# Performance work log

Measured on AMD Instinct MI355X. Metric: run time of the kernel, lower is better.

The kernel has to match this reference:

```python
import jax, jax.numpy as jnp
import numpy as np

NUM_HEADS = 8
HEAD_DIM = 64
GROUPS = 32
EPS = 1e-5


def setup_inputs() -> dict:
    key = jax.random.key(0)
    ks = jax.random.split(key, 7)
    B, C, H, W = 8, 512, 32, 32
    x = jax.random.normal(ks[0], (B, C, H, W), dtype=jnp.float32)
    gn_w = jnp.ones((C,), dtype=jnp.float32)
    gn_b = jnp.zeros((C,), dtype=jnp.float32)
    # 1x1 convs stored as [out, in] matrices
    qkv_w = jax.random.normal(ks[1], (3 * C, C), dtype=jnp.float32) * (1.0 / np.sqrt(C))
    qkv_b = jnp.zeros((3 * C,), dtype=jnp.float32)
    proj_w = jax.random.normal(ks[2], (C, C), dtype=jnp.float32) * (1.0 / np.sqrt(C))
    proj_b = jnp.zeros((C,), dtype=jnp.float32)
    return {"x": x, "gn_w": gn_w, "gn_b": gn_b, "qkv_w": qkv_w,
            "qkv_b": qkv_b, "proj_w": proj_w, "proj_b": proj_b}


def _group_norm(x, w, b):
    B, C, H, W = x.shape
    xg = x.reshape(B, GROUPS, C // GROUPS, H, W)
    mu = xg.mean(axis=(2, 3, 4), keepdims=True)
    var = xg.var(axis=(2, 3, 4), keepdims=True)
    xn = ((xg - mu) * jax.lax.rsqrt(var + EPS)).reshape(B, C, H, W)
    return xn * w[None, :, None, None] + b[None, :, None, None]


def reference(x, gn_w, gn_b, qkv_w, qkv_b, proj_w, proj_b):
    B, C, H, W = x.shape
    N = H * W
    h = _group_norm(x, gn_w, gn_b)
    # 1x1 conv == per-pixel matmul: [B, 3C, N]
    hf = h.reshape(B, C, N)
    qkv = jnp.einsum('oc,bcn->bon', qkv_w, hf) + qkv_b[None, :, None]
    qkv = qkv.reshape(B, 3, NUM_HEADS, HEAD_DIM, N)
    q, k, v = qkv[:, 0], qkv[:, 1], qkv[:, 2]  # each [B, h, d, N]
    attn = jnp.einsum('bhdi,bhdj->bhij', q, k) * (HEAD_DIM ** -0.5)
    attn = jax.nn.softmax(attn, axis=-1)
    out = jnp.einsum('bhij,bhdj->bhdi', attn, v)  # [B, h, d, N]
    out = out.reshape(B, C, N)
    out = jnp.einsum('oc,bcn->bon', proj_w, out) + proj_b[None, :, None]
    return x + out.reshape(B, C, H, W)
```

## Files before the change

### kernel.cpp

```cpp
#include <hip/hip_runtime.h>
#include <hip/hip_bf16.h>

#define BF16 __hip_bfloat16

typedef __attribute__((ext_vector_type(8))) short bf16x8;
typedef __attribute__((ext_vector_type(4))) float f32x4;
typedef __attribute__((ext_vector_type(4))) unsigned short ushort4v;
typedef __attribute__((ext_vector_type(4))) float float4v;

__device__ __forceinline__ unsigned short f2bf(float f) {
  BF16 h = __float2bfloat16(f);
  union { BF16 h; unsigned short u; } cv;
  cv.h = h;
  return cv.u;
}

__global__ __launch_bounds__(256) void cast_w_kernel(const float* __restrict__ qw,
                                                     const float* __restrict__ pw,
                                                     BF16* __restrict__ wq,
                                                     BF16* __restrict__ wp) {
  int i = blockIdx.x * 256 + threadIdx.x;
  if (i < 1536 * 512) wq[i] = __float2bfloat16(qw[i]);
  if (i < 512 * 512)  wp[i] = __float2bfloat16(pw[i]);
}

__global__ __launch_bounds__(256) void gn_kernel(const float* __restrict__ x,
                                                 const float* __restrict__ gw,
                                                 const float* __restrict__ gb,
                                                 BF16* __restrict__ h_t) {
  const int blk = blockIdx.x;
  const int bb = blk >> 5, g = blk & 31;
  const float* xg = x + (size_t)(bb * 512 + g * 16) * 1024;

  float s = 0.f, ss = 0.f;
  const float4v* x4 = (const float4v*)xg;
  for (int i = threadIdx.x; i < 4096; i += 256) {
    float4v v = x4[i];
    s  += v[0] + v[1] + v[2] + v[3];
    ss += v[0] * v[0] + v[1] * v[1] + v[2] * v[2] + v[3] * v[3];
  }
  for (int off = 32; off > 0; off >>= 1) {
    s  += __shfl_down(s, off, 64);
    ss += __shfl_down(ss, off, 64);
  }
  __shared__ float sred[8];
  const int wv = threadIdx.x >> 6;
  if ((threadIdx.x & 63) == 0) { sred[wv] = s; sred[4 + wv] = ss; }
  __syncthreads();
  const float S  = sred[0] + sred[1] + sred[2] + sred[3];
  const float SS = sred[4] + sred[5] + sred[6] + sred[7];
  const float mean = S * (1.f / 16384.f);
  const float var  = SS * (1.f / 16384.f) - mean * mean;
  const float rstd = rsqrtf(var + 1e-5f);

  const int ci = threadIdx.x & 15, nb = threadIdx.x >> 4;
  const int c  = g * 16 + ci;
  const float aw = gw[c] * rstd;
  const float ab = gb[c] - mean * aw;
  const float* xrow = xg + (size_t)ci * 1024;
  BF16* hb = h_t + (size_t)bb * 1024 * 512 + c;
  #pragma unroll 4
  for (int i = 0; i < 64; ++i) {
    int n = nb + i * 16;
    hb[(size_t)n * 512] = __float2bfloat16(aw * xrow[n] + ab);
  }
}

#define GEMM_PROLOGUE()                                                        \
  const int tid = threadIdx.x, l = tid & 63, wv = tid >> 6;                    \
  const int wm = wv >> 1, wn = wv & 1;                                         \
  const int lc = l & 15, lh = l >> 4;                                          \
  __shared__ BF16 Al[128 * 64];                                                \
  __shared__ BF16 Bl[128 * 64];                                                \
  f32x4 acc[4][4] = {};                                                        \
  for (int kt = 0; kt < 8; ++kt) {                                             \
    const int k0 = kt * 64;                                                    \
    __syncthreads();                                                           \
    _Pragma("unroll")                                                          \
    for (int it = 0; it < 4; ++it) {                                           \
      int sidx = it * 256 + tid;                                               \
      int row = sidx >> 3, cG = sidx & 7, cS = cG ^ (row & 7);                 \
      *(bf16x8*)&Al[(row * 8 + cS) * 8] =                                      \
          *(const bf16x8*)&A[(size_t)row * 512 + k0 + cG * 8];                 \
      *(bf16x8*)&Bl[(row * 8 + cS) * 8] =                                      \
          *(const bf16x8*)&B[(size_t)row * 512 + k0 + cG * 8];                 \
    }                                                                          \
    __syncthreads();                                                           \
    _Pragma("unroll")                                                          \
    for (int ks = 0; ks < 2; ++ks) {                                           \
      bf16x8 af[4], bfr[4];                                                    \
      _Pragma("unroll")                                                        \
      for (int i = 0; i < 4; ++i) {                                            \
        int rA = wm * 64 + i * 16 + lc;                                        \
        int cA = (ks * 4 + lh) ^ (rA & 7);                                     \
        af[i] = *(const bf16x8*)&Al[(rA * 8 + cA) * 8];                        \
        int rB = wn * 64 + i * 16 + lc;                                        \
        int cB = (ks * 4 + lh) ^ (rB & 7);                                     \
        bfr[i] = *(const bf16x8*)&Bl[(rB * 8 + cB) * 8];                       \
      }                                                                        \
      _Pragma("unroll")                                                        \
      for (int i = 0; i < 4; ++i)                                              \
        _Pragma("unroll")                                                      \
        for (int j = 0; j < 4; ++j)                                            \
          acc[i][j] = __builtin_amdgcn_mfma_f32_16x16x32_bf16(af[i], bfr[j],   \
                                                              acc[i][j], 0, 0, 0); \
    }                                                                          \
  }

__global__ __launch_bounds__(256) void qkv_gemm_kernel(const BF16* __restrict__ Wq,
                                                       const BF16* __restrict__ Ht,
                                                       const float* __restrict__ bias,
                                                       BF16* __restrict__ q_t,
                                                       BF16* __restrict__ k_t,
                                                       BF16* __restrict__ v_nat) {
  const int nt = blockIdx.x, mt = blockIdx.y, b = blockIdx.z;
  const int m0 = mt * 128, n0 = nt * 128;
  const BF16* A = Wq + (size_t)m0 * 512;
  const BF16* B = Ht + (size_t)b * 1024 * 512 + (size_t)n0 * 512;
  GEMM_PROLOGUE()

  const int r0 = lh * 4;
  #pragma unroll
  for (int mi = 0; mi < 4; ++mi) {
    const int o = m0 + wm * 64 + mi * 16 + r0;
    #pragma unroll
    for (int ni = 0; ni < 4; ++ni) {
      const int pix = n0 + wn * 64 + ni * 16 + lc;
      f32x4 a = acc[mi][ni];
      if (mt < 8) {
        const float scale = (mt < 4) ? 0.125f : 1.0f;
        const int hh = (o >> 6) & 7;
        const int d = o & 63;
        BF16* dst = (mt < 4 ? q_t : k_t) +
                    ((size_t)(b * 8 + hh) * 1024 + pix) * 64 + d;
        ushort4v pk;
        #pragma unroll
        for (int r = 0; r < 4; ++r) pk[r] = f2bf((a[r] + bias[o + r]) * scale);
        *(ushort4v*)dst = pk;
      } else {
        #pragma unroll
        for (int r = 0; r < 4; ++r) {
          const int vr = o + r - 1024;
          v_nat[((size_t)(b * 512 + vr)) * 1024 + pix] =
              __float2bfloat16(a[r] + bias[o + r]);
        }
      }
    }
  }
}

__global__ __launch_bounds__(256) void proj_gemm_kernel(const BF16* __restrict__ Wp,
                                                        const BF16* __restrict__ At,
                                                        const float* __restrict__ bias,
                                                        const float* __restrict__ x,
                                                        float* __restrict__ out) {
  const int nt = blockIdx.x, mt = blockIdx.y, b = blockIdx.z;
  const int m0 = mt * 128, n0 = nt * 128;
  const BF16* A = Wp + (size_t)m0 * 512;
  const BF16* B = At + (size_t)b * 1024 * 512 + (size_t)n0 * 512;
  GEMM_PROLOGUE()

  const int r0 = lh * 4;
  #pragma unroll
  for (int mi = 0; mi < 4; ++mi) {
    #pragma unroll
    for (int ni = 0; ni < 4; ++ni) {
      const int n = n0 + wn * 64 + ni * 16 + lc;
      f32x4 a = acc[mi][ni];
      #pragma unroll
      for (int r = 0; r < 4; ++r) {
        const int c = m0 + wm * 64 + mi * 16 + r0 + r;
        const size_t idx = ((size_t)(b * 512 + c)) * 1024 + n;
        out[idx] = x[idx] + bias[c] + a[r];
      }
    }
  }
}

__global__ __launch_bounds__(256) void attn_kernel(const BF16* __restrict__ q_t,
                                                   const BF16* __restrict__ k_t,
                                                   const BF16* __restrict__ v_nat,
                                                   BF16* __restrict__ attout) {
  const int bh = blockIdx.y;
  const int b = bh >> 3, hh = bh & 7;
  const int i0 = blockIdx.x * 64;
  const int tid = threadIdx.x, l = tid & 63, wv = tid >> 6;
  const int lc = l & 15, lh = l >> 4;

  __shared__ __align__(16) BF16 Kl[64 * 64];
  __shared__ __align__(16) BF16 Vl[64 * 64];
  __shared__ __align__(16) BF16 Pl[4][16][72];

  bf16x8 aq0, aq1;
  {
    const BF16* qp = q_t + ((size_t)bh * 1024 + i0 + wv * 16 + lc) * 64;
    aq0 = *(const bf16x8*)&qp[lh * 8];
    aq1 = *(const bf16x8*)&qp[32 + lh * 8];
  }

  f32x4 O[4] = {};
  float mrow[4], lrow[4];
  #pragma unroll
  for (int r = 0; r < 4; ++r) { mrow[r] = -1e30f; lrow[r] = 0.f; }

  const BF16* kbase = k_t + (size_t)bh * 1024 * 64;
  const BF16* vbase = v_nat + (size_t)bh * 64 * 1024;

  for (int jt = 0; jt < 16; ++jt) {
    const int j0 = jt * 64;
    __syncthreads();
    #pragma unroll
    for (int it = 0; it < 2; ++it) {
      int sidx = it * 256 + tid;
      int row = sidx >> 3, cG = sidx & 7, cS = cG ^ (row & 7);
      *(bf16x8*)&Kl[(row * 8 + cS) * 8] =
          *(const bf16x8*)&kbase[((size_t)(j0 + row)) * 64 + cG * 8];
      *(bf16x8*)&Vl[(row * 8 + cS) * 8] =
          *(const bf16x8*)&vbase[(size_t)row * 1024 + j0 + cG * 8];
    }
    __syncthreads();

    f32x4 Sv[4];
    #pragma unroll
    for (int jf = 0; jf < 4; ++jf) {
      f32x4 sacc = {};
      const int jl = jf * 16 + lc;
      {
        int cS = lh ^ (jl & 7);
        bf16x8 bk = *(const bf16x8*)&Kl[(jl * 8 + cS) * 8];
        sacc = __builtin_amdgcn_mfma_f32_16x16x32_bf16(aq0, bk, sacc, 0, 0, 0);
        cS = (4 + lh) ^ (jl & 7);
        bk = *(const bf16x8*)&Kl[(jl * 8 + cS) * 8];
        sacc = __builtin_amdgcn_mfma_f32_16x16x32_bf16(aq1, bk, sacc, 0, 0, 0);
      }
      Sv[jf] = sacc;
    }

    float pr[4][4];
    #pragma unroll
    for (int r = 0; r < 4; ++r) {
      float tmax = fmaxf(fmaxf(Sv[0][r], Sv[1][r]), fmaxf(Sv[2][r], Sv[3][r]));
      tmax = fmaxf(tmax, __shfl_xor(tmax, 1, 64));
      tmax = fmaxf(tmax, __shfl_xor(tmax, 2, 64));
      tmax = fmaxf(tmax, __shfl_xor(tmax, 4, 64));
      tmax = fmaxf(tmax, __shfl_xor(tmax, 8, 64));
      const float mnew = fmaxf(mrow[r], tmax);
      const float sc = __expf(mrow[r] - mnew);
      mrow[r] = mnew;
      float rs = 0.f;
      #pragma unroll
      for (int jf = 0; jf < 4; ++jf) {
        float p = __expf(Sv[jf][r] - mnew);
        pr[jf][r] = p;
        rs += p;
      }
      rs += __shfl_xor(rs, 1, 64);
      rs += __shfl_xor(rs, 2, 64);
      rs += __shfl_xor(rs, 4, 64);
      rs += __shfl_xor(rs, 8, 64);
      lrow[r] = lrow[r] * sc + rs;
      #pragma unroll
      for (int nf = 0; nf < 4; ++nf) O[nf][r] *= sc;
    }

    #pragma unroll
    for (int jf = 0; jf < 4; ++jf)
      #pragma unroll
      for (int r = 0; r < 4; ++r)
        Pl[wv][4 * lh + r][jf * 16 + lc] = __float2bfloat16(pr[jf][r]);

    const bf16x8 ap0 = *(const bf16x8*)&Pl[wv][lc][lh * 8];
    const bf16x8 ap1 = *(const bf16x8*)&Pl[wv][lc][32 + lh * 8];
    #pragma unroll
    for (int nf = 0; nf < 4; ++nf) {
      const int dl = nf * 16 + lc;
      int cS = lh ^ (dl & 7);
      bf16x8 bv = *(const bf16x8*)&Vl[(dl * 8 + cS) * 8];
      O[nf] = __builtin_amdgcn_mfma_f32_16x16x32_bf16(ap0, bv, O[nf], 0, 0, 0);
      cS = (4 + lh) ^ (dl & 7);
      bv = *(const bf16x8*)&Vl[(dl * 8 + cS) * 8];
      O[nf] = __builtin_amdgcn_mfma_f32_16x16x32_bf16(ap1, bv, O[nf], 0, 0, 0);
    }
  }

  #pragma unroll
  for (int r = 0; r < 4; ++r) {
    const float inv = 1.0f / lrow[r];
    const int irow = i0 + wv * 16 + 4 * lh + r;
    BF16* dst = attout + ((size_t)b * 1024 + irow) * 512 + hh * 64;
    #pragma unroll
    for (int nf = 0; nf < 4; ++nf)
      dst[nf * 16 + lc] = __float2bfloat16(O[nf][r] * inv);
  }
}

extern "C" void kernel_launch(void* const* d_in, const int* in_sizes, int n_in,
                              void* d_out, int out_size, void* d_ws, size_t ws_size,
                              hipStream_t stream) {
  const float* x      = (const float*)d_in[0];
  const float* gn_w   = (const float*)d_in[1];
  const float* gn_b   = (const float*)d_in[2];
  const float* qkv_w  = (const float*)d_in[3];
  const float* qkv_b  = (const float*)d_in[4];
  const float* proj_w = (const float*)d_in[5];
  const float* proj_b = (const float*)d_in[6];
  float* out = (float*)d_out;

  char* ws = (char*)d_ws;
  BF16* wq    = (BF16*)(ws);
  BF16* wp    = (BF16*)(ws + 1572864);
  BF16* h_t   = (BF16*)(ws + 2097152);
  BF16* q_t   = (BF16*)(ws + 10485760);
  BF16* k_t   = (BF16*)(ws + 18874368);
  BF16* v_nat = (BF16*)(ws + 27262976);
  BF16* attout = h_t;

  cast_w_kernel<<<3072, 256, 0, stream>>>(qkv_w, proj_w, wq, wp);
  gn_kernel<<<256, 256, 0, stream>>>(x, gn_w, gn_b, h_t);
  qkv_gemm_kernel<<<dim3(8, 12, 8), 256, 0, stream>>>(wq, h_t, qkv_b, q_t, k_t, v_nat);
  attn_kernel<<<dim3(16, 64), 256, 0, stream>>>(q_t, k_t, v_nat, attout);
  proj_gemm_kernel<<<dim3(8, 4, 8), 256, 0, stream>>>(wp, attout, proj_b, x, out);
}
```

Measured before the change: 194.0 us.

## Double-buffer attention K/V via direct global-to-LDS loads and transpose MFMA operands

GEMM and attention tile loads now use global_load_lds to write straight into LDS with the XOR swizzle applied on the global address side, skipping the register round-trip. The attention kernel double-buffers K/V so the next tile is fetched while the current one is computed. It also swaps MFMA operand order so each lane owns a whole query row: softmax needs fewer cross-lane shuffles and P and the output are written as packed 4-element stores. Risks are the ordering of the async LDS loads relative to the single barrier per iteration, and raising MFMA priority with s_setprio.

```diff
diff --git a/kernel.cpp b/kernel.cpp
--- a/kernel.cpp
+++ b/kernel.cpp
@@ -13,6 +13,12 @@
   union { BF16 h; unsigned short u; } cv;
   cv.h = h;
   return cv.u;
+}
+
+__device__ __forceinline__ void gload_lds16(const BF16* g, BF16* s) {
+  __builtin_amdgcn_global_load_lds(
+      (const __attribute__((address_space(1))) void*)g,
+      (__attribute__((address_space(3))) void*)s, 16, 0, 0);
 }
 
 __global__ __launch_bounds__(256) void cast_w_kernel(const float* __restrict__ qw,
@@ -70,20 +76,25 @@
   const int tid = threadIdx.x, l = tid & 63, wv = tid >> 6;                    \
   const int wm = wv >> 1, wn = wv & 1;                                         \
   const int lc = l & 15, lh = l >> 4;                                          \
-  __shared__ BF16 Al[128 * 64];                                                \
-  __shared__ BF16 Bl[128 * 64];                                                \
+  __shared__ __align__(16) BF16 Al[128 * 64];                                  \
+  __shared__ __align__(16) BF16 Bl[128 * 64];                                  \
   f32x4 acc[4][4] = {};                                                        \
+  int srow[4], scg[4];                                                         \
+  _Pragma("unroll")                                                            \
+  for (int t = 0; t < 4; ++t) {                                                \
+    int cidx = t * 256 + wv * 64 + l;            \
+    srow[t] = cidx >> 3;                                                       \
+    scg[t]  = (cidx & 7) ^ (srow[t] & 7);    \
+  }                                                                            \
   for (int kt = 0; kt < 8; ++kt) {                                             \
     const int k0 = kt * 64;                                                    \
     __syncthreads();                                                           \
     _Pragma("unroll")                                                          \
-    for (int it = 0; it < 4; ++it) {                                           \
-      int sidx = it * 256 + tid;                                               \
-      int row = sidx >> 3, cG = sidx & 7, cS = cG ^ (row & 7);                 \
-      *(bf16x8*)&Al[(row * 8 + cS) * 8] =                                      \
-          *(const bf16x8*)&A[(size_t)row * 512 + k0 + cG * 8];                 \
-      *(bf16x8*)&Bl[(row * 8 + cS) * 8] =                                      \
-          *(const bf16x8*)&B[(size_t)row * 512 + k0 + cG * 8];                 \
+    for (int t = 0; t < 4; ++t) {                                              \
+      gload_lds16(&A[(size_t)srow[t] * 512 + k0 + scg[t] * 8],                 \
+                  &Al[(t * 256 + wv * 64) * 8]);                               \
+      gload_lds16(&B[(size_t)srow[t] * 512 + k0 + scg[t] * 8],                 \
+                  &Bl[(t * 256 + wv * 64) * 8]);                               \
     }                                                                          \
     __syncthreads();                                                           \
     _Pragma("unroll")                                                          \
@@ -187,8 +198,8 @@
   const int tid = threadIdx.x, l = tid & 63, wv = tid >> 6;
   const int lc = l & 15, lh = l >> 4;
 
-  __shared__ __align__(16) BF16 Kl[64 * 64];
-  __shared__ __align__(16) BF16 Vl[64 * 64];
+  __shared__ __align__(16) BF16 Kl[2][64 * 64];
+  __shared__ __align__(16) BF16 Vl[2][64 * 64];
   __shared__ __align__(16) BF16 Pl[4][16][72];
 
   bf16x8 aq0, aq1;
@@ -199,98 +210,115 @@
   }
 
   f32x4 O[4] = {};
-  float mrow[4], lrow[4];
-  #pragma unroll
-  for (int r = 0; r < 4; ++r) { mrow[r] = -1e30f; lrow[r] = 0.f; }
+  float mr = -1e30f, lr = 0.f;
 
   const BF16* kbase = k_t + (size_t)bh * 1024 * 64;
   const BF16* vbase = v_nat + (size_t)bh * 64 * 1024;
 
+  int srow[2], scg[2];
+  #pragma unroll
+  for (int it = 0; it < 2; ++it) {
+    int cidx = it * 256 + wv * 64 + l;
+    srow[it] = cidx >> 3;
+    scg[it]  = (cidx & 7) ^ (srow[it] & 7);
+  }
+
+  #pragma unroll
+  for (int it = 0; it < 2; ++it) {
+    gload_lds16(&kbase[(size_t)srow[it] * 64 + scg[it] * 8],
+                &Kl[0][(it * 256 + wv * 64) * 8]);
+    gload_lds16(&vbase[(size_t)srow[it] * 1024 + scg[it] * 8],
+                &Vl[0][(it * 256 + wv * 64) * 8]);
+  }
+
   for (int jt = 0; jt < 16; ++jt) {
-    const int j0 = jt * 64;
+    const int cur = jt & 1;
     __syncthreads();
-    #pragma unroll
-    for (int it = 0; it < 2; ++it) {
-      int sidx = it * 256 + tid;
-      int row = sidx >> 3, cG = sidx & 7, cS = cG ^ (row & 7);
-      *(bf16x8*)&Kl[(row * 8 + cS) * 8] =
-          *(const bf16x8*)&kbase[((size_t)(j0 + row)) * 64 + cG * 8];
-      *(bf16x8*)&Vl[(row * 8 + cS) * 8] =
-          *(const bf16x8*)&vbase[(size_t)row * 1024 + j0 + cG * 8];
-    }
-    __syncthreads();
+    if (jt < 15) {
+      const int j1 = (jt + 1) * 64, nxt = cur ^ 1;
+      #pragma unroll
+      for (int it = 0; it < 2; ++it) {
+        gload_lds16(&kbase[(size_t)(j1 + srow[it]) * 64 + scg[it] * 8],
+                    &Kl[nxt][(it * 256 + wv * 64) * 8]);
+        gload_lds16(&vbase[(size_t)srow[it] * 1024 + j1 + scg[it] * 8],
+                    &Vl[nxt][(it * 256 + wv * 64) * 8]);
+      }
+    }
 
     f32x4 Sv[4];
+    __builtin_amdgcn_s_setprio(1);
     #pragma unroll
     for (int jf = 0; jf < 4; ++jf) {
-      f32x4 sacc = {};
       const int jl = jf * 16 + lc;
-      {
-        int cS = lh ^ (jl & 7);
-        bf16x8 bk = *(const bf16x8*)&Kl[(jl * 8 + cS) * 8];
-        sacc = __builtin_amdgcn_mfma_f32_16x16x32_bf16(aq0, bk, sacc, 0, 0, 0);
-        cS = (4 + lh) ^ (jl & 7);
-        bk = *(const bf16x8*)&Kl[(jl * 8 + cS) * 8];
-        sacc = __builtin_amdgcn_mfma_f32_16x16x32_bf16(aq1, bk, sacc, 0, 0, 0);
+      int c0 = lh ^ (jl & 7);
+      bf16x8 ak = *(const bf16x8*)&Kl[cur][(jl * 8 + c0) * 8];
+      f32x4 s0 = {};
+      s0 = __builtin_amdgcn_mfma_f32_16x16x32_bf16(ak, aq0, s0, 0, 0, 0);
+      int c1 = (4 + lh) ^ (jl & 7);
+      ak = *(const bf16x8*)&Kl[cur][(jl * 8 + c1) * 8];
+      Sv[jf] = __builtin_amdgcn_mfma_f32_16x16x32_bf16(ak, aq1, s0, 0, 0, 0);
+    }
+    __builtin_amdgcn_s_setprio(0);
+
+    float tmax = Sv[0][0];
+    #pragma unroll
+    for (int jf = 0; jf < 4; ++jf)
+      #pragma unroll
+      for (int r = 0; r < 4; ++r) tmax = fmaxf(tmax, Sv[jf][r]);
+    tmax = fmaxf(tmax, __shfl_xor(tmax, 16, 64));
+    tmax = fmaxf(tmax, __shfl_xor(tmax, 32, 64));
+    const float mnew = fmaxf(mr, tmax);
+    const float sc = __expf(mr - mnew);
+    mr = mnew;
+    float rs = 0.f;
+    float p[4][4];
+    #pragma unroll
+    for (int jf = 0; jf < 4; ++jf)
+      #pragma unroll
+      for (int r = 0; r < 4; ++r) {
+        p[jf][r] = __expf(Sv[jf][r] - mnew);
+        rs += p[jf][r];
       }
-      Sv[jf] = sacc;
-    }
-
-    float pr[4][4];
-    #pragma unroll
-    for (int r = 0; r < 4; ++r) {
-      float tmax = fmaxf(fmaxf(Sv[0][r], Sv[1][r]), fmaxf(Sv[2][r], Sv[3][r]));
-      tmax = fmaxf(tmax, __shfl_xor(tmax, 1, 64));
-      tmax = fmaxf(tmax, __shfl_xor(tmax, 2, 64));
-      tmax = fmaxf(tmax, __shfl_xor(tmax, 4, 64));
-      tmax = fmaxf(tmax, __shfl_xor(tmax, 8, 64));
-      const float mnew = fmaxf(mrow[r], tmax);
-      const float sc = __expf(mrow[r] - mnew);
-      mrow[r] = mnew;
-      float rs = 0.f;
-      #pragma unroll
-      for (int jf = 0; jf < 4; ++jf) {
-        float p = __expf(Sv[jf][r] - mnew);
-        pr[jf][r] = p;
-        rs += p;
-      }
-      rs += __shfl_xor(rs, 1, 64);
-      rs += __shfl_xor(rs, 2, 64);
-      rs += __shfl_xor(rs, 4, 64);
-      rs += __shfl_xor(rs, 8, 64);
-      lrow[r] = lrow[r] * sc + rs;
-      #pragma unroll
-      for (int nf = 0; nf < 4; ++nf) O[nf][r] *= sc;
-    }
-
-    #pragma unroll
-    for (int jf = 0; jf < 4; ++jf)
-      #pragma unroll
-      for (int r = 0; r < 4; ++r)
-        Pl[wv][4 * lh + r][jf * 16 + lc] = __float2bfloat16(pr[jf][r]);
-
-    const bf16x8 ap0 = *(const bf16x8*)&Pl[wv][lc][lh * 8];
-    const bf16x8 ap1 = *(const bf16x8*)&Pl[wv][lc][32 + lh * 8];
+    rs += __shfl_xor(rs, 16, 64);
+    rs += __shfl_xor(rs, 32, 64);
+    lr = lr * sc + rs;
+    #pragma unroll
+    for (int nf = 0; nf < 4; ++nf)
+      #pragma unroll
+      for (int r = 0; r < 4; ++r) O[nf][r] *= sc;
+
+    #pragma unroll
+    for (int jf = 0; jf < 4; ++jf) {
+      ushort4v pk;
+      #pragma unroll
+      for (int r = 0; r < 4; ++r) pk[r] = f2bf(p[jf][r]);
+      *(ushort4v*)&Pl[wv][lc][jf * 16 + 4 * lh] = pk;
+    }
+    const bf16x8 bp0 = *(const bf16x8*)&Pl[wv][lc][lh * 8];
+    const bf16x8 bp1 = *(const bf16x8*)&Pl[wv][lc][32 + lh * 8];
+
+    __builtin_amdgcn_s_setprio(1);
     #pragma unroll
     for (int nf = 0; nf < 4; ++nf) {
       const int dl = nf * 16 + lc;
-      int cS = lh ^ (dl & 7);
-      bf16x8 bv = *(const bf16x8*)&Vl[(dl * 8 + cS) * 8];
-      O[nf] = __builtin_amdgcn_mfma_f32_16x16x32_bf16(ap0, bv, O[nf], 0, 0, 0);
-      cS = (4 + lh) ^ (dl & 7);
-      bv = *(const bf16x8*)&Vl[(dl * 8 + cS) * 8];
-      O[nf] = __builtin_amdgcn_mfma_f32_16x16x32_bf16(ap1, bv, O[nf], 0, 0, 0);
-    }
-  }
-
-  #pragma unroll
-  for (int r = 0; r < 4; ++r) {
-    const float inv = 1.0f / lrow[r];
-    const int irow = i0 + wv * 16 + 4 * lh + r;
-    BF16* dst = attout + ((size_t)b * 1024 + irow) * 512 + hh * 64;
-    #pragma unroll
-    for (int nf = 0; nf < 4; ++nf)
-      dst[nf * 16 + lc] = __float2bfloat16(O[nf][r] * inv);
+      int c0 = lh ^ (dl & 7);
+      bf16x8 av = *(const bf16x8*)&Vl[cur][(dl * 8 + c0) * 8];
+      O[nf] = __builtin_amdgcn_mfma_f32_16x16x32_bf16(av, bp0, O[nf], 0, 0, 0);
+      int c1 = (4 + lh) ^ (dl & 7);
+      av = *(const bf16x8*)&Vl[cur][(dl * 8 + c1) * 8];
+      O[nf] = __builtin_amdgcn_mfma_f32_16x16x32_bf16(av, bp1, O[nf], 0, 0, 0);
+    }
+    __builtin_amdgcn_s_setprio(0);
+  }
+
+  const float inv = 1.0f / lr;
+  BF16* dst = attout + ((size_t)b * 1024 + i0 + wv * 16 + lc) * 512 + hh * 64;
+  #pragma unroll
+  for (int nf = 0; nf < 4; ++nf) {
+    ushort4v pk;
+    #pragma unroll
+    for (int r = 0; r < 4; ++r) pk[r] = f2bf(O[nf][r] * inv);
+    *(ushort4v*)&dst[nf * 16 + 4 * lh] = pk;
   }
 }
 
```

After: 184.2 us. -5.1%, faster.
